# Kernel tuning notes

Measured on AMD Instinct MI355X. Metric: run time of the kernel, lower is better.

Reference implementation:

```python
import jax, jax.numpy as jnp
import numpy as np

B, N, C_IN, C_H, C_OUT, R, X_DIM = 32, 256, 64, 128, 128, 5, 1024
NEG = -9e15

def _leaky(x, s=0.2):
    return jnp.where(x >= 0, x, s * x)

def gat_layer(atoms, mask, W, b, a):
    # atoms: (B,n,c_in), mask: (B,n,n,R) bool, W: (c_in, R*c), b: (R*c,), a: (R, 2c)
    bs, n, _ = atoms.shape
    c = a.shape[1] // 2
    h = (atoms @ W + b).reshape(bs, n, R, c)            # (B,n,R,c)
    src = jnp.einsum('bnrc,rc->bnr', h, a[:, :c])       # a . h_i part
    dst = jnp.einsum('bnrc,rc->bnr', h, a[:, c:])       # a . h_j part
    logits = _leaky(src[:, :, None, :] + dst[:, None, :, :])  # (B,i,j,R)
    masked = jnp.where(mask, logits, NEG)
    probs = jax.nn.softmax(masked.reshape(bs, n, n * R), axis=2).reshape(bs, n, n, R)
    return jnp.einsum('bijr,bjrc->bic', probs, h)       # (B,n,c)

def setup_inputs() -> dict:
    key = jax.random.key(0)
    ks = jax.random.split(key, 16)
    def p(k, shape, fan):
        return jax.random.normal(k, shape, jnp.float32) * (1.414 / np.sqrt(fan))
    inp = {
        'x': jax.random.normal(ks[0], (B, X_DIM), jnp.float32),
        'y_atoms': jax.random.normal(ks[1], (B, N, C_IN), jnp.float32),
        'y_bonds': jax.random.randint(ks[2], (B, N, N, R), 0, 2, jnp.int32),
        'W1': p(ks[3], (C_IN, R * C_H), C_IN), 'b1': jnp.zeros((R * C_H,), jnp.float32),
        'a1': p(ks[4], (R, 2 * C_H), 2 * C_H),
        'W2': p(ks[5], (C_H, R * C_H), C_H), 'b2': jnp.zeros((R * C_H,), jnp.float32),
        'a2': p(ks[6], (R, 2 * C_H), 2 * C_H),
        'W3': p(ks[7], (C_H, R * C_OUT), C_H), 'b3': jnp.zeros((R * C_OUT,), jnp.float32),
        'a3': p(ks[8], (R, 2 * C_OUT), 2 * C_OUT),
        'We1': p(ks[9], (2 * C_OUT + X_DIM, 256), 2 * C_OUT + X_DIM), 'be1': jnp.zeros((256,), jnp.float32),
        'We2': p(ks[10], (256, 32), 256), 'be2': jnp.zeros((32,), jnp.float32),
        'We3': p(ks[11], (32, 1), 32), 'be3': jnp.zeros((1,), jnp.float32),
    }
    return inp

def reference(x, y_atoms, y_bonds, W1, b1, a1, W2, b2, a2, W3, b3, a3,
              We1, be1, We2, be2, We3, be3):
    mask = (y_bonds == 1)
    h = gat_layer(y_atoms, mask, W1, b1, a1)
    h = _leaky(h)                                   # dropout is identity at eval
    h = gat_layer(h, mask, W2, b2, a2)
    h = _leaky(h)
    h = gat_layer(h, mask, W3, b3, a3)
    y_feats = jnp.concatenate([jnp.mean(h, axis=1), jnp.max(h, axis=1)], axis=1)
    z = jnp.concatenate([x, y_feats], axis=1)
    z = _leaky(z @ We1 + be1)
    z = _leaky(z @ We2 + be2)
    return z @ We3 + be3
```

## Files before the change

kernel.cpp:

```cpp
#include <hip/hip_runtime.h>
#include <cstddef>

#define BB 32
#define NN 256
#define RR 5

typedef __attribute__((ext_vector_type(8))) short bf16x8;
typedef __attribute__((ext_vector_type(4))) float f32x4;

__device__ __forceinline__ float lrelu(float x) { return x >= 0.f ? x : 0.2f * x; }
__device__ __forceinline__ unsigned short f2bf(float x) {
    unsigned u = __float_as_uint(x);
    u += 0x7FFFu + ((u >> 16) & 1u);
    return (unsigned short)(u >> 16);
}

__global__ __launch_bounds__(256) void k_prepw(const float* __restrict__ W1,
                                               const float* __restrict__ W2,
                                               const float* __restrict__ W3,
                                               const float* __restrict__ We1,
                                               unsigned short* __restrict__ WT1,
                                               unsigned short* __restrict__ WT2,
                                               unsigned short* __restrict__ WT3,
                                               float* __restrict__ We1T) {
    __shared__ float Ls[40][256];
    int blk = blockIdx.x;
    int t = threadIdx.x;
    if (blk < 30) {
        int layer = blk / 10, nt = blk % 10;
        const float* W;
        unsigned short* WT;
        int K;
        if (layer == 0)      { W = W1; WT = WT1; K = 64; }
        else if (layer == 1) { W = W2; WT = WT2; K = 128; }
        else                 { W = W3; WT = WT3; K = 128; }
        int n = nt * 64 + (t & 63);
        for (int kg = (int)(t >> 6); kg < K / 8; kg += 4) {
            bf16x8 v;
#pragma unroll
            for (int e = 0; e < 8; ++e) v[e] = (short)f2bf(W[(size_t)(kg * 8 + e) * 640 + n]);
            *(bf16x8*)&WT[(size_t)n * K + kg * 8] = v;
        }
    } else {
        int bt = blk - 30;
        for (int kk = 0; kk < 40; ++kk)
            Ls[kk][t] = We1[(size_t)(bt * 40 + kk) * 256 + t];
        __syncthreads();
#pragma unroll
        for (int q = 0; q < 10; ++q) {
            float4 v;
            v.x = Ls[q * 4 + 0][t]; v.y = Ls[q * 4 + 1][t];
            v.z = Ls[q * 4 + 2][t]; v.w = Ls[q * 4 + 3][t];
            *(float4*)&We1T[(size_t)t * 1280 + bt * 40 + q * 4] = v;
        }
    }
}

__global__ __launch_bounds__(256) void k_pack(const int* __restrict__ bonds,
                                              unsigned char* __restrict__ maskp) {
    int t = blockIdx.x * 256 + threadIdx.x;
    const int* p = bonds + (size_t)t * 5;
    unsigned m = 0;
#pragma unroll
    for (int r = 0; r < 5; ++r) m |= (p[r] == 1) ? (1u << r) : 0u;
    maskp[t] = (unsigned char)m;
}

template <int K, bool ABF16>
__global__ __launch_bounds__(256) void k_gemm_h(const float* __restrict__ Af32,
                                                const unsigned short* __restrict__ Abf,
                                                const unsigned short* __restrict__ WTg,
                                                const float* __restrict__ bias,
                                                const float* __restrict__ avec,
                                                float* __restrict__ srcp,
                                                float* __restrict__ dstp,
                                                unsigned short* __restrict__ hTf) {
    const int t = threadIdx.x;
    const int n0 = blockIdx.x * 64, m0 = blockIdx.y * 64;
    const int w = t >> 6, lane = t & 63;
    const int colg = lane & 15, rquad = lane >> 4;
    const int m = m0 + w * 16 + colg;
    const int koff = rquad * 8;

    f32x4 acc[4] = {};
#pragma unroll
    for (int kk = 0; kk < K; kk += 32) {
        bf16x8 af;
        if (ABF16) {
            af = *(const bf16x8*)&Abf[(size_t)m * K + kk + koff];
        } else {
            size_t off = (size_t)m * K + kk + koff;
            float4 q0 = *(const float4*)&Af32[off];
            float4 q1 = *(const float4*)&Af32[off + 4];
            af[0] = (short)f2bf(q0.x); af[1] = (short)f2bf(q0.y);
            af[2] = (short)f2bf(q0.z); af[3] = (short)f2bf(q0.w);
            af[4] = (short)f2bf(q1.x); af[5] = (short)f2bf(q1.y);
            af[6] = (short)f2bf(q1.z); af[7] = (short)f2bf(q1.w);
        }
#pragma unroll
        for (int ct = 0; ct < 4; ++ct) {
            bf16x8 bfv = *(const bf16x8*)&WTg[(size_t)(n0 + ct * 16 + colg) * K + kk + koff];
            acc[ct] = __builtin_amdgcn_mfma_f32_16x16x32_bf16(af, bfv, acc[ct], 0, 0, 0);
        }
    }

    const int r = n0 >> 7, chalf = n0 & 127;
    const int b = m0 >> 8, jb = m0 & 255;
    float val[4][4];
    float ssum[4] = {0.f, 0.f, 0.f, 0.f}, dsum[4] = {0.f, 0.f, 0.f, 0.f};
#pragma unroll
    for (int ct = 0; ct < 4; ++ct) {
        int cg = chalf + ct * 16 + colg;
        float bv = bias[n0 + ct * 16 + colg];
        float asr = avec[r * 256 + cg];
        float ads = avec[r * 256 + 128 + cg];
#pragma unroll
        for (int reg = 0; reg < 4; ++reg) {
            float v = acc[ct][reg] + bv;
            val[ct][reg] = v;
            ssum[reg] += v * asr;
            dsum[reg] += v * ads;
        }
    }
#pragma unroll
    for (int mk = 1; mk < 16; mk <<= 1)
#pragma unroll
        for (int reg = 0; reg < 4; ++reg) {
            ssum[reg] += __shfl_xor(ssum[reg], mk);
            dsum[reg] += __shfl_xor(dsum[reg], mk);
        }
    if (colg == 0) {
        int half = (n0 >> 6) & 1;
#pragma unroll
        for (int reg = 0; reg < 4; ++reg) {
            int row = m0 + w * 16 + rquad * 4 + reg;
            srcp[half * 40960 + row * 5 + r] = ssum[reg];
            dstp[half * 40960 + row * 5 + r] = dsum[reg];
        }
    }
    {
        const int joct = (jb >> 3) + w * 2 + (rquad >> 1);
        const size_t tile = (size_t)((b * 5 + r) * 32 + joct) * 1024;
        const int sub = (rquad & 1) * 4;
#pragma unroll
        for (int ct = 0; ct < 4; ++ct) {
            int c = chalf + ct * 16 + colg;
            uint2 pk;
            pk.x = (unsigned)f2bf(val[ct][0]) | ((unsigned)f2bf(val[ct][1]) << 16);
            pk.y = (unsigned)f2bf(val[ct][2]) | ((unsigned)f2bf(val[ct][3]) << 16);
            *(uint2*)&hTf[tile + (size_t)c * 8 + sub] = pk;
        }
    }
}

__global__ __launch_bounds__(512) void k_agg(const unsigned short* __restrict__ hTf,
                                             const float* __restrict__ srcp,
                                             const float* __restrict__ dstp,
                                             const unsigned char* __restrict__ maskp,
                                             float* __restrict__ aggP,
                                             float* __restrict__ Zpart) {
    __shared__ unsigned short Ps[20480];
    __shared__ float Ss[320], Ds2[320], Zrow[64];
    const int t = threadIdx.x;
    const int js = blockIdx.x, itile = blockIdx.y, b = blockIdx.z;
    const int i0 = itile * 64, j0 = js * 64;
    const int ib = b * 256 + i0;

    if (t < 320) Ss[t] = srcp[(size_t)ib * 5 + t] + srcp[40960 + (size_t)ib * 5 + t];
    if (t >= 320 && t < 384) Zrow[t - 320] = 0.f;
    if (t < 320) {
        int jl = t & 63, rr = t >> 6;
        size_t o = (size_t)(b * 256 + j0 + jl) * 5 + rr;
        Ds2[t] = dstp[o] + dstp[40960 + o];
    }
    __syncthreads();

#pragma unroll
    for (int it = 0; it < 5; ++it) {
        int p = it * 512 + t;
        int lane8 = p & 63, bk = p >> 6;
        int colg8 = lane8 & 15, kq = lane8 >> 4;
        int ihq = bk / 10;
        int s = bk - ihq * 10;
        int i = ihq * 16 + colg8;
        int k0 = s * 32 + kq * 8;
        int rr = k0 >> 6, jl0 = k0 & 63;
        uint2 mk8 = *(const uint2*)&maskp[((size_t)(ib + i) << 8) + j0 + jl0];
        float sv = Ss[i * 5 + rr];
        float esum = 0.f;
        bf16x8 pv;
#pragma unroll
        for (int e = 0; e < 8; ++e) {
            unsigned mb = ((e < 4 ? (mk8.x >> (8 * e)) : (mk8.y >> (8 * (e - 4)))) >> rr) & 1u;
            float v = lrelu(sv + Ds2[rr * 64 + jl0 + e]);
            float ev = mb ? __expf(v) : 0.f;
            unsigned short q = f2bf(ev);
            pv[e] = (short)q;
            esum += __uint_as_float((unsigned)q << 16);
        }
        *(bf16x8*)&Ps[p * 8] = pv;
        atomicAdd(&Zrow[i], esum);
    }
    __syncthreads();
    if (t < 64) Zpart[(size_t)js * 8192 + ib + t] = Zrow[t];

    const int w = t >> 6, lane = t & 63;
    const int ihq = w & 3, ch = w >> 2;
    const int colg = lane & 15, rquad = lane >> 4;
    f32x4 acc[4] = {};
    const size_t bbase = (size_t)(b * 5) * 32 * 1024;
#pragma unroll
    for (int s = 0; s < 10; ++s) {
        bf16x8 af = *(const bf16x8*)&Ps[((ihq * 10 + s) * 64 + lane) * 8];
        const int r = s >> 1;
        const int joct = (j0 >> 3) + (s & 1) * 4 + rquad;
        const size_t tbase = bbase + (size_t)(r * 32 + joct) * 1024;
#pragma unroll
        for (int ct = 0; ct < 4; ++ct) {
            int c = ch * 64 + ct * 16 + colg;
            bf16x8 bfv = *(const bf16x8*)&hTf[tbase + (size_t)c * 8];
            acc[ct] = __builtin_amdgcn_mfma_f32_16x16x32_bf16(af, bfv, acc[ct], 0, 0, 0);
        }
    }
    float* op = aggP + (size_t)js * 1048576;
    const int irow = ib + ihq * 16 + rquad * 4;
#pragma unroll
    for (int ct = 0; ct < 4; ++ct) {
        int c = ch * 64 + ct * 16 + colg;
#pragma unroll
        for (int reg = 0; reg < 4; ++reg)
            op[(size_t)(irow + reg) * 128 + c] = acc[ct][reg];
    }
}

__global__ __launch_bounds__(256) void k_norm(const float* __restrict__ aggP,
                                              const float* __restrict__ Zpart,
                                              unsigned short* __restrict__ Abf) {
    int idx8 = blockIdx.x * 256 + threadIdx.x;
    int row = idx8 >> 4, c0 = (idx8 & 15) * 8;
    float Z = Zpart[row] + Zpart[8192 + row] + Zpart[16384 + row] + Zpart[24576 + row];
    float zi = 1.f / Z;
    size_t o = (size_t)row * 128 + c0;
    float v[8];
#pragma unroll
    for (int h = 0; h < 2; ++h) {
        float4 s0 = *(const float4*)&aggP[o + h * 4];
        float4 s1 = *(const float4*)&aggP[o + h * 4 + 1048576];
        float4 s2 = *(const float4*)&aggP[o + h * 4 + 2097152];
        float4 s3 = *(const float4*)&aggP[o + h * 4 + 3145728];
        v[h * 4 + 0] = s0.x + s1.x + s2.x + s3.x;
        v[h * 4 + 1] = s0.y + s1.y + s2.y + s3.y;
        v[h * 4 + 2] = s0.z + s1.z + s2.z + s3.z;
        v[h * 4 + 3] = s0.w + s1.w + s2.w + s3.w;
    }
    bf16x8 ob;
#pragma unroll
    for (int e = 0; e < 8; ++e) ob[e] = (short)f2bf(lrelu(v[e] * zi));
    *(bf16x8*)&Abf[o] = ob;
}

__global__ __launch_bounds__(256) void k_pool(const float* __restrict__ aggP,
                                              const float* __restrict__ Zpart,
                                              float* __restrict__ poolS,
                                              float* __restrict__ poolM) {
    int nc = blockIdx.x, b = blockIdx.y;
    int t = threadIdx.x;
    int c = t & 127, sub = t >> 7;
    __shared__ float Zl[32];
    __shared__ float Sh[2][128], Mh[2][128];
    if (t < 32) {
        int rowg = b * 256 + nc * 32 + t;
        Zl[t] = 1.f / (Zpart[rowg] + Zpart[8192 + rowg] + Zpart[16384 + rowg] + Zpart[24576 + rowg]);
    }
    __syncthreads();
    float sm = 0.f, mx = -3.4e38f;
#pragma unroll
    for (int nn = 0; nn < 16; ++nn) {
        int nl = sub * 16 + nn;
        size_t o = (size_t)(b * 256 + nc * 32 + nl) * 128 + c;
        float v = (aggP[o] + aggP[o + 1048576] + aggP[o + 2097152] + aggP[o + 3145728]) * Zl[nl];
        sm += v; mx = fmaxf(mx, v);
    }
    Sh[sub][c] = sm; Mh[sub][c] = mx;
    __syncthreads();
    if (t < 128) {
        poolS[(b * 8 + nc) * 128 + t] = Sh[0][t] + Sh[1][t];
        poolM[(b * 8 + nc) * 128 + t] = fmaxf(Mh[0][t], Mh[1][t]);
    }
}

__global__ __launch_bounds__(256) void k_mlp1(const float* __restrict__ x,
                                              const float* __restrict__ poolS,
                                              const float* __restrict__ poolM,
                                              const float* __restrict__ We1T,
                                              const float* __restrict__ be1,
                                              float* __restrict__ z1g) {
    int og = blockIdx.x, b = blockIdx.y;
    int t = threadIdx.x;
    __shared__ float zs[1280];
    for (int i = t; i < 1024; i += 256) zs[i] = x[b * 1024 + i];
    if (t < 128) {
        float s = 0.f;
#pragma unroll
        for (int nc = 0; nc < 8; ++nc) s += poolS[(b * 8 + nc) * 128 + t];
        zs[1024 + t] = s * (1.f / 256.f);
    } else {
        int f = t - 128;
        float mx = -3.4e38f;
#pragma unroll
        for (int nc = 0; nc < 8; ++nc) mx = fmaxf(mx, poolM[(b * 8 + nc) * 128 + f]);
        zs[1152 + f] = mx;
    }
    __syncthreads();
    int w = t >> 6, lane = t & 63;
#pragma unroll
    for (int oo = 0; oo < 4; ++oo) {
        int o = og * 16 + w * 4 + oo;
        float s = 0.f;
#pragma unroll
        for (int i = 0; i < 20; ++i) {
            int k = i * 64 + lane;
            s += zs[k] * We1T[(size_t)o * 1280 + k];
        }
#pragma unroll
        for (int off = 32; off > 0; off >>= 1) s += __shfl_down(s, off);
        if (lane == 0) z1g[b * 256 + o] = lrelu(s + be1[o]);
    }
}

__global__ __launch_bounds__(256) void k_mlp23(const float* __restrict__ z1g,
                                               const float* __restrict__ We2,
                                               const float* __restrict__ be2,
                                               const float* __restrict__ We3,
                                               const float* __restrict__ be3,
                                               float* __restrict__ out) {
    int b = blockIdx.x, t = threadIdx.x;
    __shared__ float zs[256], z2s[32];
    zs[t] = z1g[b * 256 + t];
    __syncthreads();
    if (t < 32) {
        float s2 = be2[t];
        for (int k = 0; k < 256; ++k) s2 += zs[k] * We2[k * 32 + t];
        z2s[t] = lrelu(s2);
    }
    __syncthreads();
    if (t == 0) {
        float s3 = be3[0];
#pragma unroll
        for (int k = 0; k < 32; ++k) s3 += z2s[k] * We3[k];
        out[b] = s3;
    }
}

constexpr size_t O_MASK  = 0;
constexpr size_t O_SRCP  = 2097152;
constexpr size_t O_DSTP  = O_SRCP + 2ull * 40960 * 4;
constexpr size_t O_ZP    = O_DSTP + 2ull * 40960 * 4;
constexpr size_t O_AGG   = O_ZP + 4ull * 8192 * 4;
constexpr size_t O_ABF   = O_AGG + 4ull * 1048576 * 4;
constexpr size_t O_HT    = O_ABF + 1048576ull * 2;
constexpr size_t O_WT1   = O_HT + 5242880ull * 2;
constexpr size_t O_WT2   = O_WT1 + 640ull * 64 * 2;
constexpr size_t O_WT3   = O_WT2 + 640ull * 128 * 2;
constexpr size_t O_WE1T  = O_WT3 + 640ull * 128 * 2;
constexpr size_t O_POOLS = O_WE1T + 256ull * 1280 * 4;
constexpr size_t O_POOLM = O_POOLS + 32ull * 8 * 128 * 4;
constexpr size_t O_Z1    = O_POOLM + 32ull * 8 * 128 * 4;

extern "C" void kernel_launch(void* const* d_in, const int* in_sizes, int n_in,
                              void* d_out, int out_size, void* d_ws, size_t ws_size,
                              hipStream_t stream) {
    const float* x       = (const float*)d_in[0];
    const float* y_atoms = (const float*)d_in[1];
    const int*   y_bonds = (const int*)d_in[2];
    const float* W1 = (const float*)d_in[3];
    const float* b1 = (const float*)d_in[4];
    const float* a1 = (const float*)d_in[5];
    const float* W2 = (const float*)d_in[6];
    const float* b2 = (const float*)d_in[7];
    const float* a2 = (const float*)d_in[8];
    const float* W3 = (const float*)d_in[9];
    const float* b3 = (const float*)d_in[10];
    const float* a3 = (const float*)d_in[11];
    const float* We1 = (const float*)d_in[12];
    const float* be1 = (const float*)d_in[13];
    const float* We2 = (const float*)d_in[14];
    const float* be2 = (const float*)d_in[15];
    const float* We3 = (const float*)d_in[16];
    const float* be3 = (const float*)d_in[17];
    float* out = (float*)d_out;

    char* ws = (char*)d_ws;
    unsigned char* maskp = (unsigned char*)(ws + O_MASK);
    float* srcp = (float*)(ws + O_SRCP);
    float* dstp = (float*)(ws + O_DSTP);
    float* Zpart = (float*)(ws + O_ZP);
    float* aggP = (float*)(ws + O_AGG);
    unsigned short* Abf = (unsigned short*)(ws + O_ABF);
    unsigned short* hTf = (unsigned short*)(ws + O_HT);
    unsigned short* WT1 = (unsigned short*)(ws + O_WT1);
    unsigned short* WT2 = (unsigned short*)(ws + O_WT2);
    unsigned short* WT3 = (unsigned short*)(ws + O_WT3);
    float* We1T  = (float*)(ws + O_WE1T);
    float* poolS = (float*)(ws + O_POOLS);
    float* poolM = (float*)(ws + O_POOLM);
    float* z1g   = (float*)(ws + O_Z1);

    dim3 blk(256);

    k_prepw<<<62, blk, 0, stream>>>(W1, W2, W3, We1, WT1, WT2, WT3, We1T);
    k_pack<<<8192, blk, 0, stream>>>(y_bonds, maskp);

    k_gemm_h<64, false><<<dim3(10, 128), blk, 0, stream>>>(
        y_atoms, nullptr, WT1, b1, a1, srcp, dstp, hTf);
    k_agg<<<dim3(4, 4, 32), dim3(512), 0, stream>>>(hTf, srcp, dstp, maskp, aggP, Zpart);

    k_norm<<<512, blk, 0, stream>>>(aggP, Zpart, Abf);
    k_gemm_h<128, true><<<dim3(10, 128), blk, 0, stream>>>(
        nullptr, Abf, WT2, b2, a2, srcp, dstp, hTf);
    k_agg<<<dim3(4, 4, 32), dim3(512), 0, stream>>>(hTf, srcp, dstp, maskp, aggP, Zpart);

    k_norm<<<512, blk, 0, stream>>>(aggP, Zpart, Abf);
    k_gemm_h<128, true><<<dim3(10, 128), blk, 0, stream>>>(
        nullptr, Abf, WT3, b3, a3, srcp, dstp, hTf);
    k_agg<<<dim3(4, 4, 32), dim3(512), 0, stream>>>(hTf, srcp, dstp, maskp, aggP, Zpart);

    k_pool<<<dim3(8, 32), blk, 0, stream>>>(aggP, Zpart, poolS, poolM);
    k_mlp1<<<dim3(16, 32), blk, 0, stream>>>(x, poolS, poolM, We1T, be1, z1g);
    k_mlp23<<<32, blk, 0, stream>>>(z1g, We2, be2, We3, be3, out);
}
```

Before: 237.4 us.

## Fuse softmax normalization and pooling into aggregation by covering full j range per block

The aggregation kernel changes so each block handles 16 rows over all 256 neighbours. It no longer splits j into four partial sums that go to global memory, so it can normalize by the row sum in-kernel. It then writes the bf16 leaky-relu activations directly, or the per-tile sum/max pooling for the last layer. This removes the k_norm and k_pool kernels and the large aggP/Zpart round trip through HBM. The mask-packing kernel is merged into the weight-prep kernel to save a launch. The trade-off is a smaller grid with fewer, longer blocks (512 blocks of 256 threads instead of 512 blocks of 512), which may reduce parallelism.

```diff
diff --git a/kernel.cpp b/kernel.cpp
--- a/kernel.cpp
+++ b/kernel.cpp
@@ -15,14 +15,16 @@
     return (unsigned short)(u >> 16);
 }
 
-__global__ __launch_bounds__(256) void k_prepw(const float* __restrict__ W1,
-                                               const float* __restrict__ W2,
-                                               const float* __restrict__ W3,
-                                               const float* __restrict__ We1,
-                                               unsigned short* __restrict__ WT1,
-                                               unsigned short* __restrict__ WT2,
-                                               unsigned short* __restrict__ WT3,
-                                               float* __restrict__ We1T) {
+__global__ __launch_bounds__(256) void k_prep(const float* __restrict__ W1,
+                                              const float* __restrict__ W2,
+                                              const float* __restrict__ W3,
+                                              const float* __restrict__ We1,
+                                              const int* __restrict__ bonds,
+                                              unsigned short* __restrict__ WT1,
+                                              unsigned short* __restrict__ WT2,
+                                              unsigned short* __restrict__ WT3,
+                                              float* __restrict__ We1T,
+                                              unsigned char* __restrict__ maskp) {
     __shared__ float Ls[40][256];
     int blk = blockIdx.x;
     int t = threadIdx.x;
@@ -41,7 +43,7 @@
             for (int e = 0; e < 8; ++e) v[e] = (short)f2bf(W[(size_t)(kg * 8 + e) * 640 + n]);
             *(bf16x8*)&WT[(size_t)n * K + kg * 8] = v;
         }
-    } else {
+    } else if (blk < 62) {
         int bt = blk - 30;
         for (int kk = 0; kk < 40; ++kk)
             Ls[kk][t] = We1[(size_t)(bt * 40 + kk) * 256 + t];
@@ -53,17 +55,14 @@
             v.z = Ls[q * 4 + 2][t]; v.w = Ls[q * 4 + 3][t];
             *(float4*)&We1T[(size_t)t * 1280 + bt * 40 + q * 4] = v;
         }
-    }
-}
-
-__global__ __launch_bounds__(256) void k_pack(const int* __restrict__ bonds,
-                                              unsigned char* __restrict__ maskp) {
-    int t = blockIdx.x * 256 + threadIdx.x;
-    const int* p = bonds + (size_t)t * 5;
-    unsigned m = 0;
-#pragma unroll
-    for (int r = 0; r < 5; ++r) m |= (p[r] == 1) ? (1u << r) : 0u;
-    maskp[t] = (unsigned char)m;
+    } else {
+        int idx = (blk - 62) * 256 + t;
+        const int* p = bonds + (size_t)idx * 5;
+        unsigned m = 0;
+#pragma unroll
+        for (int r = 0; r < 5; ++r) m |= (p[r] == 1) ? (1u << r) : 0u;
+        maskp[idx] = (unsigned char)m;
+    }
 }
 
 template <int K, bool ABF16>
@@ -153,139 +152,107 @@
     }
 }
 
-__global__ __launch_bounds__(512) void k_agg(const unsigned short* __restrict__ hTf,
+template <bool LAST>
+__global__ __launch_bounds__(256) void k_agg(const unsigned short* __restrict__ hTf,
                                              const float* __restrict__ srcp,
                                              const float* __restrict__ dstp,
                                              const unsigned char* __restrict__ maskp,
-                                             float* __restrict__ aggP,
-                                             float* __restrict__ Zpart) {
-    __shared__ unsigned short Ps[20480];
-    __shared__ float Ss[320], Ds2[320], Zrow[64];
+                                             unsigned short* __restrict__ Abf,
+                                             float* __restrict__ poolS,
+                                             float* __restrict__ poolM) {
+    __shared__ unsigned short Ps[40 * 64 * 8];
+    __shared__ float Ss[80], Ds2[1280], Zrow[16], Zi[16];
+    __shared__ float Os[16][132];
     const int t = threadIdx.x;
-    const int js = blockIdx.x, itile = blockIdx.y, b = blockIdx.z;
-    const int i0 = itile * 64, j0 = js * 64;
-    const int ib = b * 256 + i0;
-
-    if (t < 320) Ss[t] = srcp[(size_t)ib * 5 + t] + srcp[40960 + (size_t)ib * 5 + t];
-    if (t >= 320 && t < 384) Zrow[t - 320] = 0.f;
-    if (t < 320) {
-        int jl = t & 63, rr = t >> 6;
-        size_t o = (size_t)(b * 256 + j0 + jl) * 5 + rr;
-        Ds2[t] = dstp[o] + dstp[40960 + o];
-    }
-    __syncthreads();
-
-#pragma unroll
-    for (int it = 0; it < 5; ++it) {
-        int p = it * 512 + t;
-        int lane8 = p & 63, bk = p >> 6;
-        int colg8 = lane8 & 15, kq = lane8 >> 4;
-        int ihq = bk / 10;
-        int s = bk - ihq * 10;
-        int i = ihq * 16 + colg8;
-        int k0 = s * 32 + kq * 8;
-        int rr = k0 >> 6, jl0 = k0 & 63;
-        uint2 mk8 = *(const uint2*)&maskp[((size_t)(ib + i) << 8) + j0 + jl0];
-        float sv = Ss[i * 5 + rr];
+    const int itile = blockIdx.x, b = blockIdx.y;
+    const int ib = b * 256 + itile * 16;
+
+    if (t < 80) Ss[t] = srcp[(size_t)ib * 5 + t] + srcp[40960 + (size_t)ib * 5 + t];
+    if (t >= 80 && t < 96) Zrow[t - 80] = 0.f;
+    for (int idx = t; idx < 1280; idx += 256) {
+        int jl = idx & 255, rr = idx >> 8;
+        size_t o = (size_t)(b * 256 + jl) * 5 + rr;
+        Ds2[rr * 256 + jl] = dstp[o] + dstp[40960 + o];
+    }
+    __syncthreads();
+
+    const int i_mine = t & 15;
+    {
+        float sv5[5];
+#pragma unroll
+        for (int r = 0; r < 5; ++r) sv5[r] = Ss[i_mine * 5 + r];
         float esum = 0.f;
-        bf16x8 pv;
-#pragma unroll
-        for (int e = 0; e < 8; ++e) {
-            unsigned mb = ((e < 4 ? (mk8.x >> (8 * e)) : (mk8.y >> (8 * (e - 4)))) >> rr) & 1u;
-            float v = lrelu(sv + Ds2[rr * 64 + jl0 + e]);
-            float ev = mb ? __expf(v) : 0.f;
-            unsigned short q = f2bf(ev);
-            pv[e] = (short)q;
-            esum += __uint_as_float((unsigned)q << 16);
-        }
-        *(bf16x8*)&Ps[p * 8] = pv;
-        atomicAdd(&Zrow[i], esum);
-    }
-    __syncthreads();
-    if (t < 64) Zpart[(size_t)js * 8192 + ib + t] = Zrow[t];
+#pragma unroll
+        for (int it = 0; it < 10; ++it) {
+            int p = it * 256 + t;
+            int lane8 = p & 63, s = p >> 6;
+            int kq = lane8 >> 4;
+            int k0 = s * 32 + kq * 8;
+            int rr = k0 >> 8, j0 = k0 & 255;
+            uint2 mk8 = *(const uint2*)&maskp[((size_t)(ib + i_mine) << 8) + j0];
+            float sv = sv5[rr];
+            bf16x8 pv;
+#pragma unroll
+            for (int e = 0; e < 8; ++e) {
+                unsigned mb = ((e < 4 ? (mk8.x >> (8 * e)) : (mk8.y >> (8 * (e - 4)))) >> rr) & 1u;
+                float v = lrelu(sv + Ds2[k0 + e]);
+                float ev = mb ? __expf(v) : 0.f;
+                unsigned short q = f2bf(ev);
+                pv[e] = (short)q;
+                esum += __uint_as_float((unsigned)q << 16);
+            }
+            *(bf16x8*)&Ps[p * 8] = pv;
+        }
+        atomicAdd(&Zrow[i_mine], esum);
+    }
+    __syncthreads();
+    if (t < 16) Zi[t] = 1.f / Zrow[t];
+    __syncthreads();
 
     const int w = t >> 6, lane = t & 63;
-    const int ihq = w & 3, ch = w >> 2;
     const int colg = lane & 15, rquad = lane >> 4;
-    f32x4 acc[4] = {};
+    f32x4 acc[2] = {};
     const size_t bbase = (size_t)(b * 5) * 32 * 1024;
 #pragma unroll
-    for (int s = 0; s < 10; ++s) {
-        bf16x8 af = *(const bf16x8*)&Ps[((ihq * 10 + s) * 64 + lane) * 8];
-        const int r = s >> 1;
-        const int joct = (j0 >> 3) + (s & 1) * 4 + rquad;
-        const size_t tbase = bbase + (size_t)(r * 32 + joct) * 1024;
-#pragma unroll
-        for (int ct = 0; ct < 4; ++ct) {
-            int c = ch * 64 + ct * 16 + colg;
+    for (int s = 0; s < 40; ++s) {
+        bf16x8 af = *(const bf16x8*)&Ps[(s * 64 + lane) * 8];
+        const size_t tbase = bbase + (size_t)((s >> 3) * 32 + (s & 7) * 4 + rquad) * 1024;
+#pragma unroll
+        for (int ct = 0; ct < 2; ++ct) {
+            int c = w * 32 + ct * 16 + colg;
             bf16x8 bfv = *(const bf16x8*)&hTf[tbase + (size_t)c * 8];
             acc[ct] = __builtin_amdgcn_mfma_f32_16x16x32_bf16(af, bfv, acc[ct], 0, 0, 0);
         }
     }
-    float* op = aggP + (size_t)js * 1048576;
-    const int irow = ib + ihq * 16 + rquad * 4;
-#pragma unroll
-    for (int ct = 0; ct < 4; ++ct) {
-        int c = ch * 64 + ct * 16 + colg;
-#pragma unroll
-        for (int reg = 0; reg < 4; ++reg)
-            op[(size_t)(irow + reg) * 128 + c] = acc[ct][reg];
-    }
-}
-
-__global__ __launch_bounds__(256) void k_norm(const float* __restrict__ aggP,
-                                              const float* __restrict__ Zpart,
-                                              unsigned short* __restrict__ Abf) {
-    int idx8 = blockIdx.x * 256 + threadIdx.x;
-    int row = idx8 >> 4, c0 = (idx8 & 15) * 8;
-    float Z = Zpart[row] + Zpart[8192 + row] + Zpart[16384 + row] + Zpart[24576 + row];
-    float zi = 1.f / Z;
-    size_t o = (size_t)row * 128 + c0;
-    float v[8];
-#pragma unroll
-    for (int h = 0; h < 2; ++h) {
-        float4 s0 = *(const float4*)&aggP[o + h * 4];
-        float4 s1 = *(const float4*)&aggP[o + h * 4 + 1048576];
-        float4 s2 = *(const float4*)&aggP[o + h * 4 + 2097152];
-        float4 s3 = *(const float4*)&aggP[o + h * 4 + 3145728];
-        v[h * 4 + 0] = s0.x + s1.x + s2.x + s3.x;
-        v[h * 4 + 1] = s0.y + s1.y + s2.y + s3.y;
-        v[h * 4 + 2] = s0.z + s1.z + s2.z + s3.z;
-        v[h * 4 + 3] = s0.w + s1.w + s2.w + s3.w;
-    }
-    bf16x8 ob;
-#pragma unroll
-    for (int e = 0; e < 8; ++e) ob[e] = (short)f2bf(lrelu(v[e] * zi));
-    *(bf16x8*)&Abf[o] = ob;
-}
-
-__global__ __launch_bounds__(256) void k_pool(const float* __restrict__ aggP,
-                                              const float* __restrict__ Zpart,
-                                              float* __restrict__ poolS,
-                                              float* __restrict__ poolM) {
-    int nc = blockIdx.x, b = blockIdx.y;
-    int t = threadIdx.x;
-    int c = t & 127, sub = t >> 7;
-    __shared__ float Zl[32];
-    __shared__ float Sh[2][128], Mh[2][128];
-    if (t < 32) {
-        int rowg = b * 256 + nc * 32 + t;
-        Zl[t] = 1.f / (Zpart[rowg] + Zpart[8192 + rowg] + Zpart[16384 + rowg] + Zpart[24576 + rowg]);
-    }
-    __syncthreads();
-    float sm = 0.f, mx = -3.4e38f;
-#pragma unroll
-    for (int nn = 0; nn < 16; ++nn) {
-        int nl = sub * 16 + nn;
-        size_t o = (size_t)(b * 256 + nc * 32 + nl) * 128 + c;
-        float v = (aggP[o] + aggP[o + 1048576] + aggP[o + 2097152] + aggP[o + 3145728]) * Zl[nl];
-        sm += v; mx = fmaxf(mx, v);
-    }
-    Sh[sub][c] = sm; Mh[sub][c] = mx;
-    __syncthreads();
-    if (t < 128) {
-        poolS[(b * 8 + nc) * 128 + t] = Sh[0][t] + Sh[1][t];
-        poolM[(b * 8 + nc) * 128 + t] = fmaxf(Mh[0][t], Mh[1][t]);
+    __syncthreads();
+#pragma unroll
+    for (int ct = 0; ct < 2; ++ct) {
+        int c = w * 32 + ct * 16 + colg;
+#pragma unroll
+        for (int reg = 0; reg < 4; ++reg) {
+            int i = rquad * 4 + reg;
+            Os[i][c] = acc[ct][reg] * Zi[i];
+        }
+    }
+    __syncthreads();
+
+    if (!LAST) {
+        int i = t >> 4, c0 = (t & 15) * 8;
+        bf16x8 ob;
+#pragma unroll
+        for (int e = 0; e < 8; ++e) ob[e] = (short)f2bf(lrelu(Os[i][c0 + e]));
+        *(bf16x8*)&Abf[(size_t)(ib + i) * 128 + c0] = ob;
+    } else {
+        if (t < 128) {
+            float sm = 0.f, mx = -3.4e38f;
+#pragma unroll
+            for (int i = 0; i < 16; ++i) {
+                float v = Os[i][t];
+                sm += v; mx = fmaxf(mx, v);
+            }
+            poolS[(b * 16 + itile) * 128 + t] = sm;
+            poolM[(b * 16 + itile) * 128 + t] = mx;
+        }
     }
 }
 
@@ -302,13 +269,13 @@
     if (t < 128) {
         float s = 0.f;
 #pragma unroll
-        for (int nc = 0; nc < 8; ++nc) s += poolS[(b * 8 + nc) * 128 + t];
+        for (int nc = 0; nc < 16; ++nc) s += poolS[(b * 16 + nc) * 128 + t];
         zs[1024 + t] = s * (1.f / 256.f);
     } else {
         int f = t - 128;
         float mx = -3.4e38f;
 #pragma unroll
-        for (int nc = 0; nc < 8; ++nc) mx = fmaxf(mx, poolM[(b * 8 + nc) * 128 + f]);
+        for (int nc = 0; nc < 16; ++nc) mx = fmaxf(mx, poolM[(b * 16 + nc) * 128 + f]);
         zs[1152 + f] = mx;
     }
     __syncthreads();
@@ -355,17 +322,15 @@
 constexpr size_t O_MASK  = 0;
 constexpr size_t O_SRCP  = 2097152;
 constexpr size_t O_DSTP  = O_SRCP + 2ull * 40960 * 4;
-constexpr size_t O_ZP    = O_DSTP + 2ull * 40960 * 4;
-constexpr size_t O_AGG   = O_ZP + 4ull * 8192 * 4;
-constexpr size_t O_ABF   = O_AGG + 4ull * 1048576 * 4;
+constexpr size_t O_ABF   = O_DSTP + 2ull * 40960 * 4;
 constexpr size_t O_HT    = O_ABF + 1048576ull * 2;
 constexpr size_t O_WT1   = O_HT + 5242880ull * 2;
 constexpr size_t O_WT2   = O_WT1 + 640ull * 64 * 2;
 constexpr size_t O_WT3   = O_WT2 + 640ull * 128 * 2;
 constexpr size_t O_WE1T  = O_WT3 + 640ull * 128 * 2;
 constexpr size_t O_POOLS = O_WE1T + 256ull * 1280 * 4;
-constexpr size_t O_POOLM = O_POOLS + 32ull * 8 * 128 * 4;
-constexpr size_t O_Z1    = O_POOLM + 32ull * 8 * 128 * 4;
+constexpr size_t O_POOLM = O_POOLS + 32ull * 16 * 128 * 4;
+constexpr size_t O_Z1    = O_POOLM + 32ull * 16 * 128 * 4;
 
 extern "C" void kernel_launch(void* const* d_in, const int* in_sizes, int n_in,
                               void* d_out, int out_size, void* d_ws, size_t ws_size,
@@ -394,8 +359,6 @@
     unsigned char* maskp = (unsigned char*)(ws + O_MASK);
     float* srcp = (float*)(ws + O_SRCP);
     float* dstp = (float*)(ws + O_DSTP);
-    float* Zpart = (float*)(ws + O_ZP);
-    float* aggP = (float*)(ws + O_AGG);
     unsigned short* Abf = (unsigned short*)(ws + O_ABF);
     unsigned short* hTf = (unsigned short*)(ws + O_HT);
     unsigned short* WT1 = (unsigned short*)(ws + O_WT1);
@@ -408,24 +371,20 @@
 
     dim3 blk(256);
 
-    k_prepw<<<62, blk, 0, stream>>>(W1, W2, W3, We1, WT1, WT2, WT3, We1T);
-    k_pack<<<8192, blk, 0, stream>>>(y_bonds, maskp);
+    k_prep<<<8254, blk, 0, stream>>>(W1, W2, W3, We1, y_bonds, WT1, WT2, WT3, We1T, maskp);
 
     k_gemm_h<64, false><<<dim3(10, 128), blk, 0, stream>>>(
         y_atoms, nullptr, WT1, b1, a1, srcp, dstp, hTf);
-    k_agg<<<dim3(4, 4, 32), dim3(512), 0, stream>>>(hTf, srcp, dstp, maskp, aggP, Zpart);
-
-    k_norm<<<512, blk, 0, stream>>>(aggP, Zpart, Abf);
+    k_agg<false><<<dim3(16, 32), blk, 0, stream>>>(hTf, srcp, dstp, maskp, Abf, nullptr, nullptr);
+
     k_gemm_h<128, true><<<dim3(10, 128), blk, 0, stream>>>(
         nullptr, Abf, WT2, b2, a2, srcp, dstp, hTf);
-    k_agg<<<dim3(4, 4, 32), dim3(512), 0, stream>>>(hTf, srcp, dstp, maskp, aggP, Zpart);
-
-    k_norm<<<512, blk, 0, stream>>>(aggP, Zpart, Abf);
+    k_agg<false><<<dim3(16, 32), blk, 0, stream>>>(hTf, srcp, dstp, maskp, Abf, nullptr, nullptr);
+
     k_gemm_h<128, true><<<dim3(10, 128), blk, 0, stream>>>(
         nullptr, Abf, WT3, b3, a3, srcp, dstp, hTf);
-    k_agg<<<dim3(4, 4, 32), dim3(512), 0, stream>>>(hTf, srcp, dstp, maskp, aggP, Zpart);
-
-    k_pool<<<dim3(8, 32), blk, 0, stream>>>(aggP, Zpart, poolS, poolM);
+    k_agg<true><<<dim3(16, 32), blk, 0, stream>>>(hTf, srcp, dstp, maskp, nullptr, poolS, poolM);
+
     k_mlp1<<<dim3(16, 32), blk, 0, stream>>>(x, poolS, poolM, We1T, be1, z1g);
     k_mlp23<<<32, blk, 0, stream>>>(z1g, We2, be2, We3, be3, out);
 }
```

Result: faster. 228.2 us (-3.9%).
